# Performance work log

Hardware: AMD Instinct MI355X
Metric: run time of the kernel (lower is better)

## Reference

```python
import jax, jax.numpy as jnp
import numpy as np

S = 1
R = 64
INV_T = 100.0
EVAL_STEPS = 7  # module in eval mode
EPS = 1e-6


def setup_inputs() -> dict:
    key = jax.random.key(0)
    kx, kb = jax.random.split(key)
    B, C, H, W = 8, 512, 64, 64
    x = jax.random.uniform(kx, (B, C, H, W), dtype=jnp.float32)  # non-negative input for NMF
    bases = jax.random.uniform(kb, (B * S, C // S, R), dtype=jnp.float32)
    # F.normalize(bases, dim=1): L2-normalize along D
    bases = bases / jnp.linalg.norm(bases, axis=1, keepdims=True)
    return {"x": x, "bases": bases}


def reference(x, bases):
    B, C, H, W = x.shape
    D = C // S
    N = H * W
    xf = x.reshape(B * S, D, N)  # (BS, D, N)

    # initial coefficients: softmax(inv_t * x^T @ bases)
    coef = jax.nn.softmax(INV_T * jnp.einsum('bdn,bdr->bnr', xf, bases), axis=-1)

    def mu_step(carry, _):
        bases, coef = carry
        # update coef: coef *= (x^T bases) / (coef (bases^T bases) + eps)
        num = jnp.einsum('bdn,bdr->bnr', xf, bases)            # (BS, N, R)
        gram_b = jnp.einsum('bdr,bds->brs', bases, bases)      # (BS, R, R)
        coef = coef * num / (jnp.einsum('bnr,brs->bns', coef, gram_b) + EPS)
        # update bases: bases *= (x coef) / (bases (coef^T coef) + eps)
        num_b = jnp.einsum('bdn,bnr->bdr', xf, coef)           # (BS, D, R)
        gram_c = jnp.einsum('bnr,bns->brs', coef, coef)        # (BS, R, R)
        bases = bases * num_b / (jnp.einsum('bdr,brs->bds', bases, gram_c) + EPS)
        return (bases, coef), None

    (bases, coef), _ = jax.lax.scan(mu_step, (bases, coef), None, length=EVAL_STEPS)

    # compute_coef: one extra coef multiplicative update
    num = jnp.einsum('bdn,bdr->bnr', xf, bases)
    gram_b = jnp.einsum('bdr,bds->brs', bases, bases)
    coef = coef * num / (jnp.einsum('bnr,brs->bns', coef, gram_b) + EPS)

    out = jnp.einsum('bdr,bnr->bdn', bases, coef)  # bases @ coef^T
    return out.reshape(B, C, H, W)
```

## Files before the change

kernel.cpp:

```cpp
#include <hip/hip_runtime.h>
#include <math.h>

#define BATCH 8
#define DD 512
#define NN 4096
#define RR 64
#define NSTEPS 7
#define INV_T 100.0f
#define EPSV 1e-6f
#define GC_SCALE (1.0f / 1024.0f)
#define GC_UNSCALE 1024.0f

typedef __attribute__((ext_vector_type(8))) _Float16 f16x8;
typedef __attribute__((ext_vector_type(4))) _Float16 f16x4;
typedef __attribute__((ext_vector_type(4))) float f32x4;

__device__ __forceinline__ _Float16 f2h(float f) { return (_Float16)f; }

__device__ __forceinline__ void do_xcvt(const float* x, _Float16* x_h,
                                        _Float16* xT_h, int b, int d0, int n0,
                                        int tid, char* smem) {
  _Float16(*t)[72] = (_Float16(*)[72])smem;
  const size_t xbase = (size_t)(b * DD + d0) * NN + n0;
#pragma unroll
  for (int i = 0; i < 4; ++i) {
    const int idx = tid + i * 256;
    const int row = idx >> 4, c4 = (idx & 15) * 4;
    const float4 v = *(const float4*)(x + xbase + (size_t)row * NN + c4);
    f16x4 hv = {f2h(v.x), f2h(v.y), f2h(v.z), f2h(v.w)};
    *(f16x4*)(x_h + xbase + (size_t)row * NN + c4) = hv;
    *(f16x4*)&t[row][c4] = hv;
  }
  __syncthreads();
  const size_t tbase = (size_t)(b * NN + n0) * DD + d0;
#pragma unroll
  for (int i = 0; i < 4; ++i) {
    const int idx = tid + i * 256;
    const int row = idx >> 4, c4 = (idx & 15) * 4;
    f16x4 wv = {t[c4][row], t[c4 + 1][row], t[c4 + 2][row], t[c4 + 3][row]};
    *(f16x4*)(xT_h + tbase + (size_t)row * DD + c4) = wv;
  }
}

__device__ __forceinline__ void do_bases_prep(const float* bin, float* bases32,
                                              _Float16* bases_h,
                                              _Float16* basesT_h, int b, int d0,
                                              int tid, char* smem) {
  float(*t)[65] = (float(*)[65])smem;
  const size_t base = (size_t)(b * DD + d0) * RR;
#pragma unroll
  for (int i = 0; i < 4; ++i) {
    const int idx = tid + i * 256;
    const int row = idx >> 4, c4 = (idx & 15) * 4;
    const float4 v = *(const float4*)(bin + base + row * RR + c4);
    *(float4*)(bases32 + base + row * RR + c4) = v;
    f16x4 hv = {f2h(v.x), f2h(v.y), f2h(v.z), f2h(v.w)};
    *(f16x4*)(bases_h + base + row * RR + c4) = hv;
    t[row][c4] = v.x; t[row][c4 + 1] = v.y; t[row][c4 + 2] = v.z; t[row][c4 + 3] = v.w;
  }
  __syncthreads();
#pragma unroll
  for (int i = 0; i < 4; ++i) {
    const int idx = tid + i * 256;
    const int row = idx >> 4, c4 = (idx & 15) * 4;
    f16x4 wv = {f2h(t[c4][row]), f2h(t[c4 + 1][row]), f2h(t[c4 + 2][row]),
                f2h(t[c4 + 3][row])};
    *(f16x4*)(basesT_h + (size_t)(b * RR + row) * DD + d0 + c4) = wv;
  }
}

__global__ __launch_bounds__(256) void k_gb0(const _Float16* basesT_h,
                                             _Float16* gram_b_h) {
  const int b = blockIdx.x, tid = threadIdx.x;
  const int w = tid >> 6, l = tid & 63, lo = l & 15, hi = l >> 4;
  const _Float16* ap = basesT_h + (size_t)(b * RR + w * 16 + lo) * DD + hi * 8;
  const _Float16* bp = basesT_h + (size_t)(b * RR + lo) * DD + hi * 8;
  f32x4 acc[4] = {};
#pragma unroll
  for (int ks = 0; ks < 16; ++ks) {
    f16x8 a = *(const f16x8*)(ap + ks * 32);
#pragma unroll
    for (int c = 0; c < 4; ++c) {
      f16x8 bb = *(const f16x8*)(bp + (size_t)c * 16 * DD + ks * 32);
      acc[c] = __builtin_amdgcn_mfma_f32_16x16x32_f16(a, bb, acc[c], 0, 0, 0);
    }
  }
  _Float16* op = gram_b_h + (size_t)b * 4096;
#pragma unroll
  for (int c = 0; c < 4; ++c)
#pragma unroll
    for (int r = 0; r < 4; ++r)
      op[(w * 16 + hi * 4 + r) * RR + c * 16 + lo] = f2h(acc[c][r]);
}

__global__ __launch_bounds__(256) void k_initf(const _Float16* xT_h,
                                               const _Float16* basesT_h,
                                               const _Float16* gram_b_h,
                                               _Float16* coefT_h) {
  __shared__ __attribute__((aligned(16))) _Float16 ct[64][72];
  const int tid = threadIdx.x, w = tid >> 6, l = tid & 63, lo = l & 15,
            hi = l >> 4;
  const int b = blockIdx.x >> 6, n0 = (blockIdx.x & 63) * 64;

  const _Float16* ap = xT_h + (size_t)(b * NN + n0 + w * 16 + lo) * DD + hi * 8;
  const _Float16* bp = basesT_h + (size_t)(b * RR + lo) * DD + hi * 8;
  f16x8 areg[16];
#pragma unroll
  for (int ks = 0; ks < 16; ++ks) areg[ks] = *(const f16x8*)(ap + ks * 32);
  f32x4 acc[4] = {};
#pragma unroll
  for (int ks = 0; ks < 16; ++ks) {
#pragma unroll
    for (int c = 0; c < 4; ++c) {
      f16x8 bb = *(const f16x8*)(bp + (size_t)c * 16 * DD + ks * 32);
      acc[c] = __builtin_amdgcn_mfma_f32_16x16x32_f16(areg[ks], bb, acc[c], 0, 0, 0);
    }
  }
  float v0[4][4];
#pragma unroll
  for (int reg = 0; reg < 4; ++reg) {
    float m = fmaxf(fmaxf(acc[0][reg], acc[1][reg]),
                    fmaxf(acc[2][reg], acc[3][reg]));
    m = fmaxf(m, __shfl_xor(m, 1));
    m = fmaxf(m, __shfl_xor(m, 2));
    m = fmaxf(m, __shfl_xor(m, 4));
    m = fmaxf(m, __shfl_xor(m, 8));
    float s = 0.f, e[4];
#pragma unroll
    for (int c = 0; c < 4; ++c) {
      e[c] = expf(INV_T * (acc[c][reg] - m));
      s += e[c];
    }
    s += __shfl_xor(s, 1);
    s += __shfl_xor(s, 2);
    s += __shfl_xor(s, 4);
    s += __shfl_xor(s, 8);
    const float inv = 1.f / s;
#pragma unroll
    for (int c = 0; c < 4; ++c) v0[c][reg] = e[c] * inv;
  }
#pragma unroll
  for (int reg = 0; reg < 4; ++reg)
#pragma unroll
    for (int c = 0; c < 4; ++c)
      ct[w * 16 + hi * 4 + reg][c * 16 + lo] = f2h(v0[c][reg]);
  __syncthreads();
  f32x4 den[4] = {};
#pragma unroll
  for (int kk = 0; kk < 2; ++kk) {
    f16x8 a = *(const f16x8*)&ct[w * 16 + lo][kk * 32 + hi * 8];
#pragma unroll
    for (int c = 0; c < 4; ++c) {
      f16x8 gv = *(const f16x8*)(gram_b_h + (size_t)b * 4096 +
                                 (c * 16 + lo) * RR + kk * 32 + hi * 8);
      den[c] = __builtin_amdgcn_mfma_f32_16x16x32_f16(a, gv, den[c], 0, 0, 0);
    }
  }
#pragma unroll
  for (int c = 0; c < 4; ++c) {
    f16x4 t4;
#pragma unroll
    for (int reg = 0; reg < 4; ++reg) {
      const float oldc = (float)ct[w * 16 + hi * 4 + reg][c * 16 + lo];
      t4[reg] = f2h(oldc * acc[c][reg] / (den[c][reg] + EPSV));
    }
    *(f16x4*)(coefT_h + (size_t)(b * RR + c * 16 + lo) * NN + n0 + w * 16 +
              hi * 4) = t4;
  }
}

__device__ __forceinline__ void do_coef1(const _Float16* xT_h,
                                         const _Float16* basesT_h,
                                         const float* pgb, _Float16* coefT_h,
                                         int b, int nt, int tid, int w, int lo,
                                         int hi, char* smem) {
  _Float16* gsm = (_Float16*)smem;
  _Float16(*ct)[72] = (_Float16(*)[72])(smem + 8192);
  const int n0 = nt * 64;

  const _Float16* ap = xT_h + (size_t)(b * NN + n0 + w * 16 + lo) * DD + hi * 8;
  const _Float16* bp = basesT_h + (size_t)(b * RR + lo) * DD + hi * 8;
  f16x8 areg[16];
#pragma unroll
  for (int ks = 0; ks < 16; ++ks) areg[ks] = *(const f16x8*)(ap + ks * 32);

  for (int idx = tid; idx < 4096; idx += 256) {
    float s = 0.f;
#pragma unroll
    for (int sp = 0; sp < 8; ++sp)
      s += pgb[(size_t)(b * 8 + sp) * 4096 + idx];
    gsm[idx] = f2h(s);
  }
#pragma unroll
  for (int i = 0; i < 2; ++i) {
    const int idx = tid + i * 256;
    const int r = idx >> 3, n8 = (idx & 7) * 8;
    f16x8 vv = *(const f16x8*)(coefT_h + (size_t)(b * RR + r) * NN + n0 + n8);
#pragma unroll
    for (int j = 0; j < 8; ++j) ct[n8 + j][r] = vv[j];
  }

  f32x4 acc[4] = {};
#pragma unroll
  for (int ks = 0; ks < 16; ++ks) {
#pragma unroll
    for (int c = 0; c < 4; ++c) {
      f16x8 bb = *(const f16x8*)(bp + (size_t)c * 16 * DD + ks * 32);
      acc[c] = __builtin_amdgcn_mfma_f32_16x16x32_f16(areg[ks], bb, acc[c], 0, 0, 0);
    }
  }
  __syncthreads();
  f32x4 den[4] = {};
#pragma unroll
  for (int kk = 0; kk < 2; ++kk) {
    f16x8 a = *(const f16x8*)&ct[w * 16 + lo][kk * 32 + hi * 8];
#pragma unroll
    for (int c = 0; c < 4; ++c) {
      f16x8 gv = *(const f16x8*)(gsm + (c * 16 + lo) * RR + kk * 32 + hi * 8);
      den[c] = __builtin_amdgcn_mfma_f32_16x16x32_f16(a, gv, den[c], 0, 0, 0);
    }
  }
#pragma unroll
  for (int c = 0; c < 4; ++c) {
    f16x4 t4;
#pragma unroll
    for (int reg = 0; reg < 4; ++reg) {
      const float oldc = (float)ct[w * 16 + hi * 4 + reg][c * 16 + lo];
      t4[reg] = f2h(oldc * acc[c][reg] / (den[c][reg] + EPSV));
    }
    *(f16x4*)(coefT_h + (size_t)(b * RR + c * 16 + lo) * NN + n0 + w * 16 +
              hi * 4) = t4;
  }
}

__device__ __forceinline__ void do_numb(const _Float16* x_h,
                                        const _Float16* coefT_h, float* pnb,
                                        int kc, int dt, int b, int w, int lo,
                                        int hi) {
  const _Float16* ap =
      x_h + (size_t)(b * DD + dt * 64 + w * 16 + lo) * NN + kc * 1024 + hi * 8;
  const _Float16* bp = coefT_h + (size_t)(b * RR + lo) * NN + kc * 1024 + hi * 8;
  f32x4 acc[4] = {};
#pragma unroll
  for (int half = 0; half < 2; ++half) {
    f16x8 areg[16];
#pragma unroll
    for (int ks = 0; ks < 16; ++ks)
      areg[ks] = *(const f16x8*)(ap + (half * 16 + ks) * 32);
#pragma unroll
    for (int ks = 0; ks < 16; ++ks) {
#pragma unroll
      for (int c = 0; c < 4; ++c) {
        f16x8 bb =
            *(const f16x8*)(bp + (size_t)c * 16 * NN + (half * 16 + ks) * 32);
        acc[c] =
            __builtin_amdgcn_mfma_f32_16x16x32_f16(areg[ks], bb, acc[c], 0, 0, 0);
      }
    }
  }
  float* op = pnb + ((size_t)((b * 4 + kc) * DD) + dt * 64 + w * 16 + hi * 4) * RR;
#pragma unroll
  for (int c = 0; c < 4; ++c)
#pragma unroll
    for (int r = 0; r < 4; ++r) op[r * RR + c * 16 + lo] = acc[c][r];
}

__device__ __forceinline__ void do_gramc(const _Float16* coefT_h, float* pgram,
                                         int sp, int b, int w, int lo, int hi) {
  const int k0 = sp * 256;
  const _Float16* ap = coefT_h + (size_t)(b * RR + w * 16 + lo) * NN + k0 + hi * 8;
  const _Float16* bp = coefT_h + (size_t)(b * RR + lo) * NN + k0 + hi * 8;
  f32x4 acc[4] = {};
#pragma unroll
  for (int ks = 0; ks < 8; ++ks) {
    f16x8 a = *(const f16x8*)(ap + ks * 32);
#pragma unroll
    for (int c = 0; c < 4; ++c) {
      f16x8 bb = *(const f16x8*)(bp + (size_t)c * 16 * NN + ks * 32);
      acc[c] = __builtin_amdgcn_mfma_f32_16x16x32_f16(a, bb, acc[c], 0, 0, 0);
    }
  }
  float* op = pgram + ((size_t)(b * 16 + sp) * RR + w * 16 + hi * 4) * RR;
#pragma unroll
  for (int c = 0; c < 4; ++c)
#pragma unroll
    for (int r = 0; r < 4; ++r) op[r * RR + c * 16 + lo] = acc[c][r];
}

__device__ __forceinline__ void do_bases_upd(const float* pnb,
                                             const float* pgram, float* bases32,
                                             _Float16* bases_h,
                                             _Float16* basesT_h, float* pgb,
                                             int dt, int b, int tid, int tx,
                                             int ty, char* smem) {
  float* bsm = (float*)smem;
  _Float16* gsh = (_Float16*)(smem + 16640);
  float* bg = bases32 + (size_t)(b * DD + dt * 64) * RR;
  for (int idx = tid; idx < 4096; idx += 256) {
    const int row = idx >> 6, cc = idx & 63;
    bsm[row * 65 + cc] = bg[row * 64 + cc];
  }
  for (int idx = tid; idx < 4096; idx += 256) {
    float s = 0.f;
#pragma unroll
    for (int sp = 0; sp < 16; ++sp)
      s += pgram[(size_t)(b * 16 + sp) * 4096 + idx];
    gsh[idx] = f2h(s * GC_SCALE);
  }
  __syncthreads();

  float nb[4][4];
#pragma unroll
  for (int i = 0; i < 4; ++i) {
    float4 s = make_float4(0.f, 0.f, 0.f, 0.f);
#pragma unroll
    for (int kc = 0; kc < 4; ++kc) {
      const float4 vv = *(const float4*)(pnb +
          (((size_t)b * 4 + kc) * DD + dt * 64 + ty * 4 + i) * RR + tx * 4);
      s.x += vv.x; s.y += vv.y; s.z += vv.z; s.w += vv.w;
    }
    nb[i][0] = s.x; nb[i][1] = s.y; nb[i][2] = s.z; nb[i][3] = s.w;
  }

  float den[4][4] = {};
  for (int s = 0; s < 64; ++s) {
    float a[4];
#pragma unroll
    for (int i = 0; i < 4; ++i) a[i] = bsm[(ty * 4 + i) * 65 + s];
    const f16x4 gv = *(const f16x4*)&gsh[s * 64 + tx * 4];
    const float g4[4] = {(float)gv[0], (float)gv[1], (float)gv[2], (float)gv[3]};
#pragma unroll
    for (int i = 0; i < 4; ++i)
#pragma unroll
      for (int j = 0; j < 4; ++j) den[i][j] = fmaf(a[i], g4[j], den[i][j]);
  }

  float v[4][4];
#pragma unroll
  for (int i = 0; i < 4; ++i) {
    float4 vv;
#pragma unroll
    for (int j = 0; j < 4; ++j) {
      const float oldb = bsm[(ty * 4 + i) * 65 + tx * 4 + j];
      v[i][j] = oldb * nb[i][j] / fmaf(den[i][j], GC_UNSCALE, EPSV);
    }
    vv.x = v[i][0]; vv.y = v[i][1]; vv.z = v[i][2]; vv.w = v[i][3];
    *(float4*)&bg[(ty * 4 + i) * 64 + tx * 4] = vv;
    f16x4 bv = {f2h(v[i][0]), f2h(v[i][1]), f2h(v[i][2]), f2h(v[i][3])};
    *(f16x4*)(bases_h + (size_t)(b * DD + dt * 64 + ty * 4 + i) * RR + tx * 4) = bv;
  }
#pragma unroll
  for (int j = 0; j < 4; ++j) {
    f16x4 tv = {f2h(v[0][j]), f2h(v[1][j]), f2h(v[2][j]), f2h(v[3][j])};
    *(f16x4*)(basesT_h + (size_t)(b * RR + tx * 4 + j) * DD + dt * 64 + ty * 4) = tv;
  }
  __syncthreads();
#pragma unroll
  for (int i = 0; i < 4; ++i)
#pragma unroll
    for (int j = 0; j < 4; ++j) bsm[(ty * 4 + i) * 65 + tx * 4 + j] = v[i][j];
  __syncthreads();

  float pa[4][4] = {};
  for (int d = 0; d < 64; ++d) {
    float a[4], bb[4];
#pragma unroll
    for (int i = 0; i < 4; ++i) a[i] = bsm[d * 65 + ty * 4 + i];
#pragma unroll
    for (int j = 0; j < 4; ++j) bb[j] = bsm[d * 65 + tx * 4 + j];
#pragma unroll
    for (int i = 0; i < 4; ++i)
#pragma unroll
      for (int j = 0; j < 4; ++j) pa[i][j] = fmaf(a[i], bb[j], pa[i][j]);
  }
  float* pp = pgb + (size_t)(b * 8 + dt) * 4096;
#pragma unroll
  for (int i = 0; i < 4; ++i) {
    float4 vv = make_float4(pa[i][0], pa[i][1], pa[i][2], pa[i][3]);
    *(float4*)(pp + (ty * 4 + i) * 64 + tx * 4) = vv;
  }
}

__global__ __launch_bounds__(256) void k_cout(const _Float16* xT_h,
                                              const _Float16* basesT_h,
                                              const float* pgb,
                                              const _Float16* coefT_h,
                                              const _Float16* bases_h,
                                              float* out) {
  __shared__ __attribute__((aligned(16))) char smem[17408];
  _Float16* gsm = (_Float16*)smem;
  _Float16(*ct)[72] = (_Float16(*)[72])(smem + 8192);
  const int tid = threadIdx.x, w = tid >> 6, l = tid & 63, lo = l & 15,
            hi = l >> 4;
  const int b = blockIdx.x >> 6, n0 = (blockIdx.x & 63) * 64;

  const _Float16* ap = xT_h + (size_t)(b * NN + n0 + w * 16 + lo) * DD + hi * 8;
  const _Float16* bp = basesT_h + (size_t)(b * RR + lo) * DD + hi * 8;
  f16x8 areg[16];
#pragma unroll
  for (int ks = 0; ks < 16; ++ks) areg[ks] = *(const f16x8*)(ap + ks * 32);

  for (int idx = tid; idx < 4096; idx += 256) {
    float s = 0.f;
#pragma unroll
    for (int sp = 0; sp < 8; ++sp)
      s += pgb[(size_t)(b * 8 + sp) * 4096 + idx];
    gsm[idx] = f2h(s);
  }
#pragma unroll
  for (int i = 0; i < 2; ++i) {
    const int idx = tid + i * 256;
    const int r = idx >> 3, n8 = (idx & 7) * 8;
    f16x8 vv = *(const f16x8*)(coefT_h + (size_t)(b * RR + r) * NN + n0 + n8);
#pragma unroll
    for (int j = 0; j < 8; ++j) ct[n8 + j][r] = vv[j];
  }

  f32x4 acc[4] = {};
#pragma unroll
  for (int ks = 0; ks < 16; ++ks) {
#pragma unroll
    for (int c = 0; c < 4; ++c) {
      f16x8 bb = *(const f16x8*)(bp + (size_t)c * 16 * DD + ks * 32);
      acc[c] = __builtin_amdgcn_mfma_f32_16x16x32_f16(areg[ks], bb, acc[c], 0, 0, 0);
    }
  }
  __syncthreads();
  f32x4 den[4] = {};
#pragma unroll
  for (int kk = 0; kk < 2; ++kk) {
    f16x8 a = *(const f16x8*)&ct[w * 16 + lo][kk * 32 + hi * 8];
#pragma unroll
    for (int c = 0; c < 4; ++c) {
      f16x8 gv = *(const f16x8*)(gsm + (c * 16 + lo) * RR + kk * 32 + hi * 8);
      den[c] = __builtin_amdgcn_mfma_f32_16x16x32_f16(a, gv, den[c], 0, 0, 0);
    }
  }
  float v[4][4];
#pragma unroll
  for (int c = 0; c < 4; ++c)
#pragma unroll
    for (int reg = 0; reg < 4; ++reg) {
      const float oldc = (float)ct[w * 16 + hi * 4 + reg][c * 16 + lo];
      v[c][reg] = oldc * acc[c][reg] / (den[c][reg] + EPSV);
    }
  __syncthreads();
#pragma unroll
  for (int c = 0; c < 4; ++c)
#pragma unroll
    for (int reg = 0; reg < 4; ++reg)
      ct[w * 16 + hi * 4 + reg][c * 16 + lo] = f2h(v[c][reg]);
  __syncthreads();

  for (int dt = 0; dt < 8; ++dt) {
    const _Float16* bap =
        bases_h + (size_t)(b * DD + dt * 64 + w * 16 + lo) * RR + hi * 8;
    f32x4 oacc[4] = {};
#pragma unroll
    for (int kk = 0; kk < 2; ++kk) {
      f16x8 a = *(const f16x8*)(bap + kk * 32);
#pragma unroll
      for (int c = 0; c < 4; ++c) {
        f16x8 bb = *(const f16x8*)&ct[c * 16 + lo][kk * 32 + hi * 8];
        oacc[c] = __builtin_amdgcn_mfma_f32_16x16x32_f16(a, bb, oacc[c], 0, 0, 0);
      }
    }
    float* op = out + (size_t)(b * DD + dt * 64 + w * 16 + hi * 4) * NN + n0;
#pragma unroll
    for (int c = 0; c < 4; ++c)
#pragma unroll
      for (int r = 0; r < 4; ++r) op[(size_t)r * NN + c * 16 + lo] = oacc[c][r];
  }
}

__global__ __launch_bounds__(256) void k_out(const _Float16* bases_h,
                                             const _Float16* coefT_h,
                                             float* out) {
  __shared__ __attribute__((aligned(16))) _Float16 ct[64][72];
  const int tid = threadIdx.x, w = tid >> 6, l = tid & 63, lo = l & 15,
            hi = l >> 4;
  const int nt = blockIdx.x, dt = blockIdx.y, b = blockIdx.z;
  const int n0 = nt * 64;
#pragma unroll
  for (int i = 0; i < 2; ++i) {
    const int idx = tid + i * 256;
    const int r = idx >> 3, n8 = (idx & 7) * 8;
    f16x8 vv = *(const f16x8*)(coefT_h + (size_t)(b * RR + r) * NN + n0 + n8);
#pragma unroll
    for (int j = 0; j < 8; ++j) ct[n8 + j][r] = vv[j];
  }
  __syncthreads();
  const _Float16* ap =
      bases_h + (size_t)(b * DD + dt * 64 + w * 16 + lo) * RR + hi * 8;
  f32x4 acc[4] = {};
#pragma unroll
  for (int kk = 0; kk < 2; ++kk) {
    f16x8 a = *(const f16x8*)(ap + kk * 32);
#pragma unroll
    for (int c = 0; c < 4; ++c) {
      f16x8 bb = *(const f16x8*)&ct[c * 16 + lo][kk * 32 + hi * 8];
      acc[c] = __builtin_amdgcn_mfma_f32_16x16x32_f16(a, bb, acc[c], 0, 0, 0);
    }
  }
  float* op = out + (size_t)(b * DD + dt * 64 + w * 16 + hi * 4) * NN + n0;
#pragma unroll
  for (int c = 0; c < 4; ++c)
#pragma unroll
    for (int r = 0; r < 4; ++r) op[(size_t)r * NN + c * 16 + lo] = acc[c][r];
}

__global__ __launch_bounds__(256) void k_prep(const float* x, const float* bin,
                                              float* b32, _Float16* x_h,
                                              _Float16* xT_h, _Float16* bh,
                                              _Float16* bth) {
  __shared__ __attribute__((aligned(16))) char smem[16640];
  const int g = blockIdx.x, tid = threadIdx.x;
  if (g < 4096)
    do_xcvt(x, x_h, xT_h, g >> 9, ((g >> 6) & 7) * 64, (g & 63) * 64, tid, smem);
  else {
    const int q = g - 4096;
    do_bases_prep(bin, b32, bh, bth, q >> 3, (q & 7) * 64, tid, smem);
  }
}
__global__ __launch_bounds__(256) void k_coef1(const _Float16* xT_h,
                                               const _Float16* basesT_h,
                                               const float* pgb,
                                               _Float16* coefT_h) {
  __shared__ __attribute__((aligned(16))) char smem[17408];
  const int tid = threadIdx.x, w = tid >> 6, l = tid & 63, lo = l & 15,
            hi = l >> 4;
  do_coef1(xT_h, basesT_h, pgb, coefT_h, blockIdx.x >> 6, blockIdx.x & 63, tid,
           w, lo, hi, smem);
}
__global__ __launch_bounds__(256) void k_nbgc(const _Float16* x_h,
                                              const _Float16* coefT_h,
                                              float* pnb, float* pgram) {
  const int tid = threadIdx.x, w = tid >> 6, l = tid & 63, lo = l & 15,
            hi = l >> 4;
  const int g = blockIdx.x;
  if (g < 256)
    do_numb(x_h, coefT_h, pnb, g & 3, (g >> 2) & 7, g >> 5, w, lo, hi);
  else {
    const int q = g - 256;
    do_gramc(coefT_h, pgram, q & 15, q >> 4, w, lo, hi);
  }
}
__global__ __launch_bounds__(256) void k_bupd(const float* pnb,
                                              const float* pgram, float* b32,
                                              _Float16* bh, _Float16* bth,
                                              float* pgb) {
  __shared__ __attribute__((aligned(16))) char smem[24832];
  do_bases_upd(pnb, pgram, b32, bh, bth, pgb, blockIdx.x & 7, blockIdx.x >> 3,
               threadIdx.x, threadIdx.x & 15, threadIdx.x >> 4, smem);
}

extern "C" void kernel_launch(void* const* d_in, const int* in_sizes, int n_in,
                              void* d_out, int out_size, void* d_ws,
                              size_t ws_size, hipStream_t stream) {
  (void)in_sizes; (void)n_in; (void)out_size;
  const float* x = (const float*)d_in[0];
  const float* bin = (const float*)d_in[1];
  float* W = (float*)d_ws;
  float* O = (float*)d_out;

  float* bases32 = W;
  float* pnb = bases32 + 262144;
  float* pgram = pnb + 1048576;
  float* pgb = pgram + 524288;
  _Float16* coefT_h = (_Float16*)(pgb + 262144);
  _Float16* bases_h = coefT_h + 2097152;
  _Float16* basesT_h = bases_h + 262144;
  _Float16* gram_b_h = basesT_h + 262144;
  _Float16* ws_end = gram_b_h + 32768;

  const size_t xhalves = (size_t)BATCH * NN * DD;
  const size_t need = ((char*)(ws_end + 2 * xhalves)) - (char*)W;
  _Float16* xT_h;
  _Float16* x_h;
  const bool ws_fits = (ws_size >= need);
  if (ws_fits) {
    xT_h = ws_end;
    x_h = xT_h + xhalves;
  } else {
    xT_h = (_Float16*)O;
    x_h = xT_h + xhalves;
  }

  k_prep<<<4160, 256, 0, stream>>>(x, bin, bases32, x_h, xT_h, bases_h,
                                   basesT_h);
  k_gb0<<<BATCH, 256, 0, stream>>>(basesT_h, gram_b_h);
  k_initf<<<512, 256, 0, stream>>>(xT_h, basesT_h, gram_b_h, coefT_h);
  for (int s = 0; s < NSTEPS; ++s) {
    k_nbgc<<<384, 256, 0, stream>>>(x_h, coefT_h, pnb, pgram);
    k_bupd<<<64, 256, 0, stream>>>(pnb, pgram, bases32, bases_h, basesT_h, pgb);
    if (s < NSTEPS - 1)
      k_coef1<<<512, 256, 0, stream>>>(xT_h, basesT_h, pgb, coefT_h);
  }
  if (ws_fits) {
    k_cout<<<512, 256, 0, stream>>>(xT_h, basesT_h, pgb, coefT_h, bases_h, O);
  } else {
    k_coef1<<<512, 256, 0, stream>>>(xT_h, basesT_h, pgb, coefT_h);
    k_out<<<dim3(64, 8, BATCH), 256, 0, stream>>>(bases_h, coefT_h, O);
  }
}
```

Measured before the change: 543.8 us.

## Reduce gram_b partials in a separate kernel and stream A-fragments per k-step

Adds a small k_gb kernel that sums the eight partial bases Gram matrices once per batch into an fp16 buffer. Previously each of the 512 coef-update blocks redid this reduction into shared memory. The coef and output kernels now read the reduced Gram matrix directly from global memory, which also shrinks their shared memory. The GEMM loops in initf, coef1, cout and numb now load A fragments per k-step instead of preloading 16 into registers, lowering register pressure at the cost of less load-ahead latency hiding, and the extra kernel launch per step adds overhead.

```diff
diff --git a/kernel.cpp b/kernel.cpp
--- a/kernel.cpp
+++ b/kernel.cpp
@@ -93,6 +93,20 @@
       op[(w * 16 + hi * 4 + r) * RR + c * 16 + lo] = f2h(acc[c][r]);
 }
 
+__global__ __launch_bounds__(256) void k_gb(const float* pgb,
+                                            _Float16* gram_b_h) {
+  const int b = blockIdx.x >> 3;
+  const int e0 = (blockIdx.x & 7) * 512 + threadIdx.x;
+#pragma unroll
+  for (int t = 0; t < 2; ++t) {
+    const int e = e0 + t * 256;
+    float s = 0.f;
+#pragma unroll
+    for (int sp = 0; sp < 8; ++sp) s += pgb[(size_t)(b * 8 + sp) * 4096 + e];
+    gram_b_h[(size_t)b * 4096 + e] = f2h(s);
+  }
+}
+
 __global__ __launch_bounds__(256) void k_initf(const _Float16* xT_h,
                                                const _Float16* basesT_h,
                                                const _Float16* gram_b_h,
@@ -104,16 +118,14 @@
 
   const _Float16* ap = xT_h + (size_t)(b * NN + n0 + w * 16 + lo) * DD + hi * 8;
   const _Float16* bp = basesT_h + (size_t)(b * RR + lo) * DD + hi * 8;
-  f16x8 areg[16];
-#pragma unroll
-  for (int ks = 0; ks < 16; ++ks) areg[ks] = *(const f16x8*)(ap + ks * 32);
   f32x4 acc[4] = {};
 #pragma unroll
   for (int ks = 0; ks < 16; ++ks) {
+    f16x8 a = *(const f16x8*)(ap + ks * 32);
 #pragma unroll
     for (int c = 0; c < 4; ++c) {
       f16x8 bb = *(const f16x8*)(bp + (size_t)c * 16 * DD + ks * 32);
-      acc[c] = __builtin_amdgcn_mfma_f32_16x16x32_f16(areg[ks], bb, acc[c], 0, 0, 0);
+      acc[c] = __builtin_amdgcn_mfma_f32_16x16x32_f16(a, bb, acc[c], 0, 0, 0);
     }
   }
   float v0[4][4];
@@ -171,42 +183,31 @@
 
 __device__ __forceinline__ void do_coef1(const _Float16* xT_h,
                                          const _Float16* basesT_h,
-                                         const float* pgb, _Float16* coefT_h,
-                                         int b, int nt, int tid, int w, int lo,
-                                         int hi, char* smem) {
-  _Float16* gsm = (_Float16*)smem;
-  _Float16(*ct)[72] = (_Float16(*)[72])(smem + 8192);
+                                         const _Float16* gram_b_h,
+                                         _Float16* coefT_h, int b, int nt,
+                                         int tid, int w, int lo, int hi,
+                                         char* smem) {
+  _Float16(*ct)[72] = (_Float16(*)[72])smem;
   const int n0 = nt * 64;
+#pragma unroll
+  for (int i = 0; i < 2; ++i) {
+    const int idx = tid + i * 256;
+    const int r = idx >> 3, n8 = (idx & 7) * 8;
+    f16x8 vv = *(const f16x8*)(coefT_h + (size_t)(b * RR + r) * NN + n0 + n8);
+#pragma unroll
+    for (int j = 0; j < 8; ++j) ct[n8 + j][r] = vv[j];
+  }
 
   const _Float16* ap = xT_h + (size_t)(b * NN + n0 + w * 16 + lo) * DD + hi * 8;
   const _Float16* bp = basesT_h + (size_t)(b * RR + lo) * DD + hi * 8;
-  f16x8 areg[16];
-#pragma unroll
-  for (int ks = 0; ks < 16; ++ks) areg[ks] = *(const f16x8*)(ap + ks * 32);
-
-  for (int idx = tid; idx < 4096; idx += 256) {
-    float s = 0.f;
-#pragma unroll
-    for (int sp = 0; sp < 8; ++sp)
-      s += pgb[(size_t)(b * 8 + sp) * 4096 + idx];
-    gsm[idx] = f2h(s);
-  }
-#pragma unroll
-  for (int i = 0; i < 2; ++i) {
-    const int idx = tid + i * 256;
-    const int r = idx >> 3, n8 = (idx & 7) * 8;
-    f16x8 vv = *(const f16x8*)(coefT_h + (size_t)(b * RR + r) * NN + n0 + n8);
-#pragma unroll
-    for (int j = 0; j < 8; ++j) ct[n8 + j][r] = vv[j];
-  }
-
   f32x4 acc[4] = {};
 #pragma unroll
   for (int ks = 0; ks < 16; ++ks) {
+    f16x8 a = *(const f16x8*)(ap + ks * 32);
 #pragma unroll
     for (int c = 0; c < 4; ++c) {
       f16x8 bb = *(const f16x8*)(bp + (size_t)c * 16 * DD + ks * 32);
-      acc[c] = __builtin_amdgcn_mfma_f32_16x16x32_f16(areg[ks], bb, acc[c], 0, 0, 0);
+      acc[c] = __builtin_amdgcn_mfma_f32_16x16x32_f16(a, bb, acc[c], 0, 0, 0);
     }
   }
   __syncthreads();
@@ -216,7 +217,8 @@
     f16x8 a = *(const f16x8*)&ct[w * 16 + lo][kk * 32 + hi * 8];
 #pragma unroll
     for (int c = 0; c < 4; ++c) {
-      f16x8 gv = *(const f16x8*)(gsm + (c * 16 + lo) * RR + kk * 32 + hi * 8);
+      f16x8 gv = *(const f16x8*)(gram_b_h + (size_t)b * 4096 +
+                                 (c * 16 + lo) * RR + kk * 32 + hi * 8);
       den[c] = __builtin_amdgcn_mfma_f32_16x16x32_f16(a, gv, den[c], 0, 0, 0);
     }
   }
@@ -241,21 +243,13 @@
       x_h + (size_t)(b * DD + dt * 64 + w * 16 + lo) * NN + kc * 1024 + hi * 8;
   const _Float16* bp = coefT_h + (size_t)(b * RR + lo) * NN + kc * 1024 + hi * 8;
   f32x4 acc[4] = {};
-#pragma unroll
-  for (int half = 0; half < 2; ++half) {
-    f16x8 areg[16];
-#pragma unroll
-    for (int ks = 0; ks < 16; ++ks)
-      areg[ks] = *(const f16x8*)(ap + (half * 16 + ks) * 32);
-#pragma unroll
-    for (int ks = 0; ks < 16; ++ks) {
-#pragma unroll
-      for (int c = 0; c < 4; ++c) {
-        f16x8 bb =
-            *(const f16x8*)(bp + (size_t)c * 16 * NN + (half * 16 + ks) * 32);
-        acc[c] =
-            __builtin_amdgcn_mfma_f32_16x16x32_f16(areg[ks], bb, acc[c], 0, 0, 0);
-      }
+#pragma unroll 4
+  for (int ks = 0; ks < 32; ++ks) {
+    f16x8 a = *(const f16x8*)(ap + ks * 32);
+#pragma unroll
+    for (int c = 0; c < 4; ++c) {
+      f16x8 bb = *(const f16x8*)(bp + (size_t)c * 16 * NN + ks * 32);
+      acc[c] = __builtin_amdgcn_mfma_f32_16x16x32_f16(a, bb, acc[c], 0, 0, 0);
     }
   }
   float* op = pnb + ((size_t)((b * 4 + kc) * DD) + dt * 64 + w * 16 + hi * 4) * RR;
@@ -383,46 +377,34 @@
 
 __global__ __launch_bounds__(256) void k_cout(const _Float16* xT_h,
                                               const _Float16* basesT_h,
-                                              const float* pgb,
+                                              const _Float16* gram_b_h,
                                               const _Float16* coefT_h,
                                               const _Float16* bases_h,
                                               float* out) {
-  __shared__ __attribute__((aligned(16))) char smem[17408];
-  _Float16* gsm = (_Float16*)smem;
-  _Float16(*ct)[72] = (_Float16(*)[72])(smem + 8192);
+  __shared__ __attribute__((aligned(16))) _Float16 ct[64][72];
   const int tid = threadIdx.x, w = tid >> 6, l = tid & 63, lo = l & 15,
             hi = l >> 4;
   const int b = blockIdx.x >> 6, n0 = (blockIdx.x & 63) * 64;
 
+#pragma unroll
+  for (int i = 0; i < 2; ++i) {
+    const int idx = tid + i * 256;
+    const int r = idx >> 3, n8 = (idx & 7) * 8;
+    f16x8 vv = *(const f16x8*)(coefT_h + (size_t)(b * RR + r) * NN + n0 + n8);
+#pragma unroll
+    for (int j = 0; j < 8; ++j) ct[n8 + j][r] = vv[j];
+  }
+
   const _Float16* ap = xT_h + (size_t)(b * NN + n0 + w * 16 + lo) * DD + hi * 8;
   const _Float16* bp = basesT_h + (size_t)(b * RR + lo) * DD + hi * 8;
-  f16x8 areg[16];
-#pragma unroll
-  for (int ks = 0; ks < 16; ++ks) areg[ks] = *(const f16x8*)(ap + ks * 32);
-
-  for (int idx = tid; idx < 4096; idx += 256) {
-    float s = 0.f;
-#pragma unroll
-    for (int sp = 0; sp < 8; ++sp)
-      s += pgb[(size_t)(b * 8 + sp) * 4096 + idx];
-    gsm[idx] = f2h(s);
-  }
-#pragma unroll
-  for (int i = 0; i < 2; ++i) {
-    const int idx = tid + i * 256;
-    const int r = idx >> 3, n8 = (idx & 7) * 8;
-    f16x8 vv = *(const f16x8*)(coefT_h + (size_t)(b * RR + r) * NN + n0 + n8);
-#pragma unroll
-    for (int j = 0; j < 8; ++j) ct[n8 + j][r] = vv[j];
-  }
-
   f32x4 acc[4] = {};
 #pragma unroll
   for (int ks = 0; ks < 16; ++ks) {
+    f16x8 a = *(const f16x8*)(ap + ks * 32);
 #pragma unroll
     for (int c = 0; c < 4; ++c) {
       f16x8 bb = *(const f16x8*)(bp + (size_t)c * 16 * DD + ks * 32);
-      acc[c] = __builtin_amdgcn_mfma_f32_16x16x32_f16(areg[ks], bb, acc[c], 0, 0, 0);
+      acc[c] = __builtin_amdgcn_mfma_f32_16x16x32_f16(a, bb, acc[c], 0, 0, 0);
     }
   }
   __syncthreads();
@@ -432,7 +414,8 @@
     f16x8 a = *(const f16x8*)&ct[w * 16 + lo][kk * 32 + hi * 8];
 #pragma unroll
     for (int c = 0; c < 4; ++c) {
-      f16x8 gv = *(const f16x8*)(gsm + (c * 16 + lo) * RR + kk * 32 + hi * 8);
+      f16x8 gv = *(const f16x8*)(gram_b_h + (size_t)b * 4096 +
+                                 (c * 16 + lo) * RR + kk * 32 + hi * 8);
       den[c] = __builtin_amdgcn_mfma_f32_16x16x32_f16(a, gv, den[c], 0, 0, 0);
     }
   }
@@ -524,13 +507,13 @@
 }
 __global__ __launch_bounds__(256) void k_coef1(const _Float16* xT_h,
                                                const _Float16* basesT_h,
-                                               const float* pgb,
+                                               const _Float16* gram_b_h,
                                                _Float16* coefT_h) {
-  __shared__ __attribute__((aligned(16))) char smem[17408];
+  __shared__ __attribute__((aligned(16))) char smem[9216];
   const int tid = threadIdx.x, w = tid >> 6, l = tid & 63, lo = l & 15,
             hi = l >> 4;
-  do_coef1(xT_h, basesT_h, pgb, coefT_h, blockIdx.x >> 6, blockIdx.x & 63, tid,
-           w, lo, hi, smem);
+  do_coef1(xT_h, basesT_h, gram_b_h, coefT_h, blockIdx.x >> 6, blockIdx.x & 63,
+           tid, w, lo, hi, smem);
 }
 __global__ __launch_bounds__(256) void k_nbgc(const _Float16* x_h,
                                               const _Float16* coefT_h,
@@ -593,13 +576,15 @@
   for (int s = 0; s < NSTEPS; ++s) {
     k_nbgc<<<384, 256, 0, stream>>>(x_h, coefT_h, pnb, pgram);
     k_bupd<<<64, 256, 0, stream>>>(pnb, pgram, bases32, bases_h, basesT_h, pgb);
+    k_gb<<<64, 256, 0, stream>>>(pgb, gram_b_h);
     if (s < NSTEPS - 1)
-      k_coef1<<<512, 256, 0, stream>>>(xT_h, basesT_h, pgb, coefT_h);
+      k_coef1<<<512, 256, 0, stream>>>(xT_h, basesT_h, gram_b_h, coefT_h);
   }
   if (ws_fits) {
-    k_cout<<<512, 256, 0, stream>>>(xT_h, basesT_h, pgb, coefT_h, bases_h, O);
+    k_cout<<<512, 256, 0, stream>>>(xT_h, basesT_h, gram_b_h, coefT_h, bases_h,
+                                    O);
   } else {
-    k_coef1<<<512, 256, 0, stream>>>(xT_h, basesT_h, pgb, coefT_h);
+    k_coef1<<<512, 256, 0, stream>>>(xT_h, basesT_h, gram_b_h, coefT_h);
     k_out<<<dim3(64, 8, BATCH), 256, 0, stream>>>(bases_h, coefT_h, O);
   }
 }
```

Result: faster. 524.5 us (-3.5%).
